# Kernel tuning notes

Hardware: AMD Instinct MI355X
Metric: run time of the kernel (lower is better)

## Reference

```python
import jax, jax.numpy as jnp
import numpy as np

K_NN = 64          # ume_knn
RADIUS = 1.5       # ume_desc_rad
EPS_M = 1e-6
EPS_T = 1e-16


def ball_query_idx(kp, pts, K, radius):
    # kp: [bs, n_kp, 3], pts: [bs, N, 3] -> idx [bs, n_kp, K], -1 padded
    N = pts.shape[1]
    d2 = jnp.sum((kp[:, :, None, :] - pts[:, None, :, :]) ** 2, axis=-1)  # [bs,n_kp,N]
    mask = d2 < radius ** 2
    cand = jnp.where(mask, jnp.arange(N, dtype=jnp.int32), N)
    order = jnp.sort(cand, axis=-1)[..., :K]          # first K in-ball indices (by point index)
    return jnp.where(order == N, -1, order)


def ball_query_gather(pts, idx):
    # pad row 0 with zeros so idx=-1 gathers zeros (matches torch ball_query_gather)
    bs = pts.shape[0]
    padded = jnp.concatenate([jnp.zeros((bs, 1, pts.shape[-1]), pts.dtype), pts], axis=1)
    return padded[jnp.arange(bs)[:, None, None], idx + 1]  # [bs, n_kp, K, D]


def ume_mat(points, features):
    # points: [B', K, 3], features: [B', K, F] -> [B', F, 4]
    m0 = jnp.sum(features, axis=1)                       # [B', F]
    m1 = jnp.einsum('bkf,bkd->bfd', features, points)    # [B', F, 3]
    um = jnp.concatenate([m0[:, :, None], m1], axis=2)   # [B', F, 4]
    denom = jnp.sum(m0, axis=-1)[:, None, None] + EPS_M  # [B',1,1]
    return um / denom


def batch_estimate_transform_ume(G, H):
    # G, H: [B, F, 4]
    mg, mh = G[:, :, 0:1], H[:, :, 0:1]                  # [B,F,1]
    g, h = G[:, :, 1:], H[:, :, 1:]                      # [B,F,3]
    mg_sq = jnp.sum(mg ** 2, axis=1, keepdims=True) + EPS_T
    mg_mh = jnp.sum(mg * mh, axis=1, keepdims=True)
    gmg = jnp.sum(g * mg, axis=1, keepdims=True)         # [B,1,3]
    hmg = jnp.sum(h * mg, axis=1, keepdims=True)
    wlc = gmg / (mg_sq + EPS_T)
    wrc = hmg / (mg_mh + EPS_T)
    left = g - wlc * mg
    right = h - wrc * mh
    M = jnp.einsum('bfi,bfj->bij', right, left)          # right^T @ left, [B,3,3]
    U, S, VH = jnp.linalg.svd(jnp.swapaxes(M, 1, 2))
    sgn = jnp.sign(jnp.linalg.det(U @ VH))
    qd = jnp.stack([jnp.ones_like(sgn), jnp.ones_like(sgn), sgn], axis=-1)  # diag(1,1,sgn)
    R = (U * qd[:, None, :]) @ VH                        # [B,3,3]
    b2 = (wrc - wlc @ R)[:, 0, :]                        # [B,3]
    H_orth = jnp.linalg.qr(H, mode='reduced')[0]
    G_orth = jnp.linalg.qr(G, mode='reduced')[0]
    diff = H_orth @ jnp.swapaxes(H_orth, 1, 2) - G_orth @ jnp.swapaxes(G_orth, 1, 2)
    D = 0.707 * jnp.sqrt(jnp.sum(diff ** 2, axis=(1, 2)))
    top = jnp.concatenate([jnp.swapaxes(R, 1, 2), b2[:, :, None]], axis=2)  # [B,3,4]
    bottom = jnp.broadcast_to(jnp.array([[0.0, 0.0, 0.0, 1.0]], G.dtype), (G.shape[0], 1, 4))
    T = jnp.concatenate([top, bottom], axis=1)           # [B,4,4]
    return T, D


def setup_inputs() -> dict:
    key = jax.random.key(0)
    ks = jax.random.split(key, 6)
    bs, N, F, n_kp = 2, 16384, 64, 64
    return {
        'source_points': jax.random.normal(ks[0], (bs, N, 3), jnp.float32),
        'source_features': jax.random.uniform(ks[1], (bs, N, F), jnp.float32),
        'source_kp': jax.random.normal(ks[2], (bs, n_kp, 3), jnp.float32),
        'target_points': jax.random.normal(ks[3], (bs, N, 3), jnp.float32),
        'target_features': jax.random.uniform(ks[4], (bs, N, F), jnp.float32),
        'target_kp': jax.random.normal(ks[5], (bs, n_kp, 3), jnp.float32),
    }


def reference(source_points, source_features, source_kp, target_points, target_features, target_kp):
    bs, n_kp = source_kp.shape[0], source_kp.shape[1]
    F = source_features.shape[-1]
    s_idx = ball_query_idx(source_kp, source_points, K_NN, RADIUS)
    t_idx = ball_query_idx(target_kp, target_points, K_NN, RADIUS)
    s_pts = ball_query_gather(source_points, s_idx).reshape(bs * n_kp, K_NN, 3)
    s_ft = ball_query_gather(source_features, s_idx).reshape(bs * n_kp, K_NN, F)
    t_pts = ball_query_gather(target_points, t_idx).reshape(bs * n_kp, K_NN, 3)
    t_ft = ball_query_gather(target_features, t_idx).reshape(bs * n_kp, K_NN, F)
    G_kp = ume_mat(s_pts, s_ft).reshape(bs, n_kp, F, 4)[:, :, None]   # [bs,n_kp,1,F,4]
    H_kp = ume_mat(t_pts, t_ft).reshape(bs, n_kp, F, 4)[:, None]      # [bs,1,n_kp,F,4]
    G = jnp.broadcast_to(G_kp, (bs, n_kp, n_kp, F, 4)).reshape(-1, F, 4)
    H = jnp.broadcast_to(H_kp, (bs, n_kp, n_kp, F, 4)).reshape(-1, F, 4)
    T, D = batch_estimate_transform_ume(G, H)
    T = T.reshape(bs, n_kp, n_kp, 4, 4)
    D = D.reshape(bs, n_kp, n_kp)
    return T, D, jnp.squeeze(G_kp), jnp.squeeze(H_kp)
```

## Files before the change

kernel.cpp:

```cpp
#include <hip/hip_runtime.h>
#include <math.h>

#define N_PTS 16384
#define N_KP  64
#define NF    64
#define KNN   64
#define NWAVE 16

#define OFF_T 0
#define OFF_D 131072
#define OFF_G 139264
#define OFF_H 172032

__device__ __forceinline__ float wsum(float v) {
  #pragma unroll
  for (int m = 1; m < 64; m <<= 1) v += __shfl_xor(v, m, 64);
  return v;
}

__global__ __launch_bounds__(1024) void ume_stage1(
    const float* __restrict__ sp, const float* __restrict__ sf, const float* __restrict__ skp,
    const float* __restrict__ tp, const float* __restrict__ tf, const float* __restrict__ tkp,
    float* __restrict__ out, double* __restrict__ rec)
{
  const int kp = blockIdx.x, b = blockIdx.y, side = blockIdx.z;
  const int tid  = threadIdx.x;
  const int lane = tid & 63;
  const int w    = tid >> 6;
  const float* pts  = side ? tp  : sp;
  const float* feat = side ? tf  : sf;
  const float* kps  = side ? tkp : skp;

  const float kx = kps[(b*N_KP + kp)*3 + 0];
  const float ky = kps[(b*N_KP + kp)*3 + 1];
  const float kz = kps[(b*N_KP + kp)*3 + 2];

  __shared__ int   s_widx[NWAVE*KNN];
  __shared__ int   s_wcount[NWAVE];
  __shared__ int   s_woff[NWAVE];
  __shared__ int   s_total;
  __shared__ int   s_final[KNN];
  __shared__ float s_px[KNN], s_py[KNN], s_pz[KNN];
  __shared__ float s_m0[NWAVE][NF], s_mx[NWAVE][NF], s_my[NWAVE][NF], s_mz[NWAVE][NF];

  float px[16], py[16], pz[16];
  const size_t pbase = ((size_t)b*N_PTS + w*1024 + lane)*3;
  #pragma unroll
  for (int k = 0; k < 16; ++k) {
    const float* pp = pts + pbase + (size_t)k*64*3;
    px[k] = pp[0]; py[k] = pp[1]; pz[k] = pp[2];
  }
  int running = 0;
  #pragma unroll
  for (int k = 0; k < 16; ++k) {
    const float dx = px[k]-kx, dy = py[k]-ky, dz = pz[k]-kz;
    const bool hit = (dx*dx + dy*dy + dz*dz) < 2.25f;
    const unsigned long long m = __ballot(hit);
    if (hit) {
      const int pos = running + __popcll(m & ((1ull<<lane)-1ull));
      if (pos < KNN) s_widx[w*KNN + pos] = w*1024 + k*64 + lane;
    }
    running += (int)__popcll(m);
  }
  if (lane == 0) s_wcount[w] = running > KNN ? KNN : running;
  __syncthreads();

  if (tid < NWAVE) {
    int off = 0;
    for (int q = 0; q < tid; ++q) off += s_wcount[q];
    s_woff[tid] = off;
    if (tid == NWAVE-1) {
      int tot = off + s_wcount[tid];
      s_total = tot > KNN ? KNN : tot;
    }
  }
  __syncthreads();

  {
    const int e = tid & 63, ww = tid >> 6;
    if (e < s_wcount[ww]) {
      const int slot = s_woff[ww] + e;
      if (slot < KNN) s_final[slot] = s_widx[ww*KNN + e];
    }
  }
  __syncthreads();

  const int total = s_total;
  if (tid < KNN && tid < total) {
    const float* pp = pts + ((size_t)b*N_PTS + s_final[tid])*3;
    s_px[tid] = pp[0]; s_py[tid] = pp[1]; s_pz[tid] = pp[2];
  }
  __syncthreads();

  {
    const int f = tid & 63, g = tid >> 6;
    float m0 = 0.f, mxv = 0.f, myv = 0.f, mzv = 0.f;
    for (int k = g; k < total; k += NWAVE) {
      const float fv = feat[((size_t)b*N_PTS + s_final[k])*NF + f];
      m0  += fv;
      mxv += fv * s_px[k];
      myv += fv * s_py[k];
      mzv += fv * s_pz[k];
    }
    s_m0[g][f] = m0; s_mx[g][f] = mxv; s_my[g][f] = myv; s_mz[g][f] = mzv;
  }
  __syncthreads();

  if (tid >= 64) return;

  float m0 = 0.f, mxv = 0.f, myv = 0.f, mzv = 0.f;
  #pragma unroll
  for (int g = 0; g < NWAVE; ++g) {
    m0  += s_m0[g][lane];
    mxv += s_mx[g][lane];
    myv += s_my[g][lane];
    mzv += s_mz[g][lane];
  }
  const float denom = wsum(m0) + 1e-6f;
  float u[4];
  u[0] = m0/denom; u[1] = mxv/denom; u[2] = myv/denom; u[3] = mzv/denom;

  float* dst = out + (side ? OFF_H : OFF_G) + ((size_t)(b*N_KP+kp)*NF + lane)*4;
  dst[0]=u[0]; dst[1]=u[1]; dst[2]=u[2]; dst[3]=u[3];

  float A[4][4];
  #pragma unroll
  for (int c = 0; c < 4; ++c)
    #pragma unroll
    for (int d = c; d < 4; ++d) {
      const float s = wsum(u[c]*u[d]);
      A[c][d] = s; A[d][c] = s;
    }

  if (lane < 16)
    rec[(size_t)((side*2 + b)*N_KP + kp)*16 + lane] = (double)A[lane>>2][lane&3];
}

__device__ __forceinline__ void cof_inv4(const double A[4][4], double Ai[4][4], double sc[4]) {
  #pragma unroll
  for (int c = 0; c < 4; ++c) sc[c] = 1.0/sqrt(fmax(A[c][c], 1e-300));
  double M[4][4];
  #pragma unroll
  for (int r = 0; r < 4; ++r)
    #pragma unroll
    for (int c = 0; c < 4; ++c) M[r][c] = A[r][c]*sc[r]*sc[c];
  const double s0 = M[0][0]*M[1][1] - M[0][1]*M[1][0];
  const double s1 = M[0][0]*M[1][2] - M[0][2]*M[1][0];
  const double s2 = M[0][0]*M[1][3] - M[0][3]*M[1][0];
  const double s3 = M[0][1]*M[1][2] - M[0][2]*M[1][1];
  const double s4 = M[0][1]*M[1][3] - M[0][3]*M[1][1];
  const double s5 = M[0][2]*M[1][3] - M[0][3]*M[1][2];
  const double c5 = M[2][2]*M[3][3] - M[2][3]*M[3][2];
  const double c4 = M[2][1]*M[3][3] - M[2][3]*M[3][1];
  const double c3 = M[2][1]*M[3][2] - M[2][2]*M[3][1];
  const double c2 = M[2][0]*M[3][3] - M[2][3]*M[3][0];
  const double c1 = M[2][0]*M[3][2] - M[2][2]*M[3][0];
  const double c0 = M[2][0]*M[3][1] - M[2][1]*M[3][0];
  const double det = s0*c5 - s1*c4 + s2*c3 + s3*c2 - s4*c1 + s5*c0;
  const double invd = 1.0/fmax(det, 1e-300);
  Ai[0][0] = ( M[1][1]*c5 - M[1][2]*c4 + M[1][3]*c3)*invd;
  Ai[0][1] = (-M[0][1]*c5 + M[0][2]*c4 - M[0][3]*c3)*invd;
  Ai[0][2] = ( M[3][1]*s5 - M[3][2]*s4 + M[3][3]*s3)*invd;
  Ai[0][3] = (-M[2][1]*s5 + M[2][2]*s4 - M[2][3]*s3)*invd;
  Ai[1][0] = (-M[1][0]*c5 + M[1][2]*c2 - M[1][3]*c1)*invd;
  Ai[1][1] = ( M[0][0]*c5 - M[0][2]*c2 + M[0][3]*c1)*invd;
  Ai[1][2] = (-M[3][0]*s5 + M[3][2]*s2 - M[3][3]*s1)*invd;
  Ai[1][3] = ( M[2][0]*s5 - M[2][2]*s2 + M[2][3]*s1)*invd;
  Ai[2][0] = ( M[1][0]*c4 - M[1][1]*c2 + M[1][3]*c0)*invd;
  Ai[2][1] = (-M[0][0]*c4 + M[0][1]*c2 - M[0][3]*c0)*invd;
  Ai[2][2] = ( M[3][0]*s4 - M[3][1]*s2 + M[3][3]*s0)*invd;
  Ai[2][3] = (-M[2][0]*s4 + M[2][1]*s2 - M[2][3]*s0)*invd;
  Ai[3][0] = (-M[1][0]*c3 + M[1][1]*c1 - M[1][2]*c0)*invd;
  Ai[3][1] = ( M[0][0]*c3 - M[0][1]*c1 + M[0][2]*c0)*invd;
  Ai[3][2] = (-M[3][0]*s3 + M[3][1]*s1 - M[3][2]*s0)*invd;
  Ai[3][3] = ( M[2][0]*s3 - M[2][1]*s1 + M[2][2]*s0)*invd;
}

__global__ __launch_bounds__(256) void ume_stage2(
    const float* __restrict__ gh, float* __restrict__ out,
    const double* __restrict__ rec)
{
  const int q  = blockIdx.x*256 + threadIdx.x;
  const int b2 = q >> 12;
  const int i  = (q >> 6) & 63;
  const int j  = q & 63;

  const float4* Gp = (const float4*)(gh + OFF_G) + (size_t)(b2*N_KP + i)*NF;
  const float4* Hp = (const float4*)(gh + OFF_H) + (size_t)(b2*N_KP + j)*NF;

  double X[4][4] = {};
  for (int f = 0; f < NF; ++f) {
    const float4 g = Gp[f];
    const float4 h = Hp[f];
    const double gc[4] = {(double)g.x, (double)g.y, (double)g.z, (double)g.w};
    const double hc[4] = {(double)h.x, (double)h.y, (double)h.z, (double)h.w};
    #pragma unroll
    for (int c = 0; c < 4; ++c)
      #pragma unroll
      for (int d = 0; d < 4; ++d)
        X[c][d] += hc[c]*gc[d];
  }

  double Ag[4][4], Bh[4][4];
  {
    const double* pg = rec + (size_t)(b2*N_KP + i)*16;
    const double* ph = rec + (size_t)((2 + b2)*N_KP + j)*16;
    #pragma unroll
    for (int k = 0; k < 16; ++k) { Ag[k>>2][k&3] = pg[k]; Bh[k>>2][k&3] = ph[k]; }
  }
  double Aig[4][4], scg[4], Bih[4][4], sch[4];
  cof_inv4(Ag, Aig, scg);
  cof_inv4(Bh, Bih, sch);

  const double inv_dwl = 1.0/(Ag[0][0] + 2e-16);
  const double wl[3] = {Ag[0][1]*inv_dwl, Ag[0][2]*inv_dwl, Ag[0][3]*inv_dwl};
  const double inv_dmm = 1.0/(X[0][0] + 1e-16);
  const double wr[3] = {X[1][0]*inv_dmm, X[2][0]*inv_dmm, X[3][0]*inv_dmm};

  double M3[3][3];
  #pragma unroll
  for (int r = 0; r < 3; ++r)
    #pragma unroll
    for (int c = 0; c < 3; ++c)
      M3[r][c] = X[1+r][1+c] - wl[c]*X[1+r][0] - wr[r]*X[0][1+c] + wr[r]*wl[c]*X[0][0];

  double C[3][3];
  for (int r = 0; r < 3; ++r)
    for (int c = 0; c < 3; ++c) C[r][c] = M3[c][r];

  double mmax = 0.0;
  for (int r = 0; r < 3; ++r)
    for (int c = 0; c < 3; ++c) mmax = fmax(mmax, fabs(C[r][c]));

  double R[3][3] = {{1,0,0},{0,1,0},{0,0,1}};
  if (mmax > 1e-300) {
    const double is = 1.0/mmax;
    for (int r = 0; r < 3; ++r)
      for (int c = 0; c < 3; ++c) C[r][c] *= is;
    double K[3][3];
    for (int p = 0; p < 3; ++p)
      for (int qq = 0; qq < 3; ++qq) {
        double s = 0.0;
        for (int r = 0; r < 3; ++r) s += C[r][p]*C[r][qq];
        K[p][qq] = s;
      }
    double V[3][3] = {{1,0,0},{0,1,0},{0,0,1}};
    for (int sweep = 0; sweep < 5; ++sweep) {
      for (int p = 0; p < 2; ++p)
        for (int qq = p+1; qq < 3; ++qq) {
          const double apq = K[p][qq];
          if (apq*apq < 1e-26) continue;
          const double tau = (K[qq][qq] - K[p][p])/(2.0*apq);
          const double t   = (tau >= 0.0 ? 1.0 : -1.0)/(fabs(tau) + sqrt(1.0 + tau*tau));
          const double cth = 1.0/sqrt(1.0 + t*t);
          const double sth = t*cth;
          for (int k = 0; k < 3; ++k) {
            const double a = K[p][k], bb_ = K[qq][k];
            K[p][k] = cth*a - sth*bb_;
            K[qq][k] = sth*a + cth*bb_;
          }
          for (int k = 0; k < 3; ++k) {
            const double a = K[k][p], bb_ = K[k][qq];
            K[k][p] = cth*a - sth*bb_;
            K[k][qq] = sth*a + cth*bb_;
          }
          for (int k = 0; k < 3; ++k) {
            const double a = V[k][p], bb_ = V[k][qq];
            V[k][p] = cth*a - sth*bb_;
            V[k][qq] = sth*a + cth*bb_;
          }
        }
    }
    int o0 = 0, o1 = 1, o2 = 2;
    double e0 = K[0][0], e1 = K[1][1], e2 = K[2][2];
    if (e0 < e1) { double te=e0; e0=e1; e1=te; int to=o0; o0=o1; o1=to; }
    if (e0 < e2) { double te=e0; e0=e2; e2=te; int to=o0; o0=o2; o2=to; }
    if (e1 < e2) { double te=e1; e1=e2; e2=te; int to=o1; o1=o2; o2=to; }
    (void)e0; (void)e1; (void)e2;
    double v1[3] = {V[0][o0], V[1][o0], V[2][o0]};
    double v2[3] = {V[0][o1], V[1][o1], V[2][o1]};
    double u1[3], u2[3];
    for (int r = 0; r < 3; ++r) u1[r] = C[r][0]*v1[0] + C[r][1]*v1[1] + C[r][2]*v1[2];
    const double n1 = sqrt(u1[0]*u1[0] + u1[1]*u1[1] + u1[2]*u1[2]);
    if (n1 > 1e-150) { const double rn = 1.0/n1; u1[0]*=rn; u1[1]*=rn; u1[2]*=rn; }
    else             { u1[0]=1.0; u1[1]=0.0; u1[2]=0.0; }
    for (int r = 0; r < 3; ++r) u2[r] = C[r][0]*v2[0] + C[r][1]*v2[1] + C[r][2]*v2[2];
    const double d12 = u2[0]*u1[0] + u2[1]*u1[1] + u2[2]*u1[2];
    for (int r = 0; r < 3; ++r) u2[r] -= d12*u1[r];
    const double n2 = sqrt(u2[0]*u2[0] + u2[1]*u2[1] + u2[2]*u2[2]);
    if (n2 > 1e-100) { const double rn = 1.0/n2; u2[0]*=rn; u2[1]*=rn; u2[2]*=rn; }
    else {
      double t0, t1, t2;
      if (fabs(u1[0]) < 0.9) { t0=1.0; t1=0.0; t2=0.0; } else { t0=0.0; t1=1.0; t2=0.0; }
      const double dd = t0*u1[0] + t1*u1[1] + t2*u1[2];
      u2[0]=t0-dd*u1[0]; u2[1]=t1-dd*u1[1]; u2[2]=t2-dd*u1[2];
      const double nn = 1.0/sqrt(u2[0]*u2[0] + u2[1]*u2[1] + u2[2]*u2[2]);
      u2[0]*=nn; u2[1]*=nn; u2[2]*=nn;
    }
    const double u3[3] = {u1[1]*u2[2]-u1[2]*u2[1], u1[2]*u2[0]-u1[0]*u2[2], u1[0]*u2[1]-u1[1]*u2[0]};
    const double v3[3] = {v1[1]*v2[2]-v1[2]*v2[1], v1[2]*v2[0]-v1[0]*v2[2], v1[0]*v2[1]-v1[1]*v2[0]};
    for (int r = 0; r < 3; ++r)
      for (int c = 0; c < 3; ++c)
        R[r][c] = u1[r]*v1[c] + u2[r]*v2[c] + u3[r]*v3[c];
  }

  double bb[3];
  for (int d = 0; d < 3; ++d)
    bb[d] = wr[d] - (wl[0]*R[0][d] + wl[1]*R[1][d] + wl[2]*R[2][d]);

  double Xh[4][4];
  for (int c = 0; c < 4; ++c)
    for (int d = 0; d < 4; ++d) Xh[c][d] = X[c][d]*sch[c]*scg[d];
  double W[4][4];
  for (int r = 0; r < 4; ++r)
    for (int c = 0; c < 4; ++c) {
      double s = 0.0;
      for (int k = 0; k < 4; ++k) s += Bih[r][k]*Xh[k][c];
      W[r][c] = s;
    }
  double tr = 0.0;
  for (int r = 0; r < 4; ++r)
    for (int c = 0; c < 4; ++c) {
      double s = 0.0;
      for (int k = 0; k < 4; ++k) s += W[r][k]*Aig[k][c];
      tr += s*Xh[r][c];
    }
  const double Dv = 0.707*sqrt(fmax(8.0 - 2.0*tr, 0.0));

  float* tptr = out + OFF_T + (size_t)((b2*N_KP + i)*N_KP + j)*16;
  tptr[0]=(float)R[0][0];  tptr[1]=(float)R[1][0];  tptr[2]=(float)R[2][0];  tptr[3]=(float)bb[0];
  tptr[4]=(float)R[0][1];  tptr[5]=(float)R[1][1];  tptr[6]=(float)R[2][1];  tptr[7]=(float)bb[1];
  tptr[8]=(float)R[0][2];  tptr[9]=(float)R[1][2];  tptr[10]=(float)R[2][2]; tptr[11]=(float)bb[2];
  tptr[12]=0.f; tptr[13]=0.f; tptr[14]=0.f; tptr[15]=1.f;

  out[OFF_D + (size_t)(b2*N_KP + i)*N_KP + j] = (float)Dv;
}

extern "C" void kernel_launch(void* const* d_in, const int* in_sizes, int n_in,
                              void* d_out, int out_size, void* d_ws, size_t ws_size,
                              hipStream_t stream) {
  const float* sp  = (const float*)d_in[0];
  const float* sf  = (const float*)d_in[1];
  const float* skp = (const float*)d_in[2];
  const float* tp  = (const float*)d_in[3];
  const float* tf  = (const float*)d_in[4];
  const float* tkp = (const float*)d_in[5];
  float* out = (float*)d_out;
  double* rec = (double*)d_ws;

  dim3 gA(N_KP, 2, 2);
  ume_stage1<<<gA, 1024, 0, stream>>>(sp, sf, skp, tp, tf, tkp, out, rec);
  ume_stage2<<<32, 256, 0, stream>>>(out, out, rec);
}
```

Measured before the change: 98.43 us.

## Precompute per-keypoint 4x4 inverses once and tile stage2 into 8x8 pair blocks

Moves the two cofactor 4x4 inversions and the wl weights out of every (i,j) pair thread into a small ume_invert kernel that runs once per keypoint and stores the results in workspace. Stage2 then reads these precomputed records instead of redoing the inversions 64 times each. Stage2 also changes from 32 blocks of 256 threads to 128 blocks of 64 threads covering 8x8 pair tiles, which spreads work over more CUs and lets G/H rows be reused within a block. The cost is an extra kernel launch and a serial dependency, plus extra global reads of the double records.

```diff
diff --git a/kernel.cpp b/kernel.cpp
--- a/kernel.cpp
+++ b/kernel.cpp
@@ -11,6 +11,8 @@
 #define OFF_D 131072
 #define OFF_G 139264
 #define OFF_H 172032
+
+#define REC2_OFF 4096
 
 __device__ __forceinline__ float wsum(float v) {
   #pragma unroll
@@ -176,17 +178,38 @@
   Ai[3][3] = ( M[2][0]*s3 - M[2][1]*s1 + M[2][2]*s0)*invd;
 }
 
-__global__ __launch_bounds__(256) void ume_stage2(
+__global__ __launch_bounds__(64) void ume_invert(double* __restrict__ ws)
+{
+  const int t = blockIdx.x*64 + threadIdx.x;
+  if (t >= 256) return;
+  const double* pa = ws + (size_t)t*16;
+  double A[4][4];
+  #pragma unroll
+  for (int k = 0; k < 16; ++k) A[k>>2][k&3] = pa[k];
+  double Ai[4][4], sc[4];
+  cof_inv4(A, Ai, sc);
+  double* rp = ws + REC2_OFF + (size_t)t*24;
+  #pragma unroll
+  for (int k = 0; k < 16; ++k) rp[k] = Ai[k>>2][k&3];
+  rp[16]=sc[0]; rp[17]=sc[1]; rp[18]=sc[2]; rp[19]=sc[3];
+  const double inv_dwl = 1.0/(A[0][0] + 2e-16);
+  rp[20] = A[0][1]*inv_dwl;
+  rp[21] = A[0][2]*inv_dwl;
+  rp[22] = A[0][3]*inv_dwl;
+  rp[23] = 0.0;
+}
+
+__global__ __launch_bounds__(64) void ume_stage2(
     const float* __restrict__ gh, float* __restrict__ out,
-    const double* __restrict__ rec)
+    const double* __restrict__ rec2)
 {
-  const int q  = blockIdx.x*256 + threadIdx.x;
-  const int b2 = q >> 12;
-  const int i  = (q >> 6) & 63;
-  const int j  = q & 63;
-
-  const float4* Gp = (const float4*)(gh + OFF_G) + (size_t)(b2*N_KP + i)*NF;
-  const float4* Hp = (const float4*)(gh + OFF_H) + (size_t)(b2*N_KP + j)*NF;
+  const int jt = blockIdx.x, it = blockIdx.y, b = blockIdx.z;
+  const int lane = threadIdx.x;
+  const int i = it*8 + (lane >> 3);
+  const int j = jt*8 + (lane & 7);
+
+  const float4* Gp = (const float4*)(gh + OFF_G) + (size_t)(b*N_KP + i)*NF;
+  const float4* Hp = (const float4*)(gh + OFF_H) + (size_t)(b*N_KP + j)*NF;
 
   double X[4][4] = {};
   for (int f = 0; f < NF; ++f) {
@@ -201,32 +224,23 @@
         X[c][d] += hc[c]*gc[d];
   }
 
-  double Ag[4][4], Bh[4][4];
-  {
-    const double* pg = rec + (size_t)(b2*N_KP + i)*16;
-    const double* ph = rec + (size_t)((2 + b2)*N_KP + j)*16;
-    #pragma unroll
-    for (int k = 0; k < 16; ++k) { Ag[k>>2][k&3] = pg[k]; Bh[k>>2][k&3] = ph[k]; }
-  }
-  double Aig[4][4], scg[4], Bih[4][4], sch[4];
-  cof_inv4(Ag, Aig, scg);
-  cof_inv4(Bh, Bih, sch);
-
-  const double inv_dwl = 1.0/(Ag[0][0] + 2e-16);
-  const double wl[3] = {Ag[0][1]*inv_dwl, Ag[0][2]*inv_dwl, Ag[0][3]*inv_dwl};
+  const double* rg = rec2 + (size_t)(b*N_KP + i)*24;
+  const double* rh = rec2 + (size_t)((2 + b)*N_KP + j)*24;
+
+  const double wl[3] = {rg[20], rg[21], rg[22]};
   const double inv_dmm = 1.0/(X[0][0] + 1e-16);
   const double wr[3] = {X[1][0]*inv_dmm, X[2][0]*inv_dmm, X[3][0]*inv_dmm};
 
-  double M3[3][3];
+  double M[3][3];
   #pragma unroll
   for (int r = 0; r < 3; ++r)
     #pragma unroll
     for (int c = 0; c < 3; ++c)
-      M3[r][c] = X[1+r][1+c] - wl[c]*X[1+r][0] - wr[r]*X[0][1+c] + wr[r]*wl[c]*X[0][0];
+      M[r][c] = X[1+r][1+c] - wl[c]*X[1+r][0] - wr[r]*X[0][1+c] + wr[r]*wl[c]*X[0][0];
 
   double C[3][3];
   for (int r = 0; r < 3; ++r)
-    for (int c = 0; c < 3; ++c) C[r][c] = M3[c][r];
+    for (int c = 0; c < 3; ++c) C[r][c] = M[c][r];
 
   double mmax = 0.0;
   for (int r = 0; r < 3; ++r)
@@ -239,35 +253,35 @@
       for (int c = 0; c < 3; ++c) C[r][c] *= is;
     double K[3][3];
     for (int p = 0; p < 3; ++p)
-      for (int qq = 0; qq < 3; ++qq) {
+      for (int q = 0; q < 3; ++q) {
         double s = 0.0;
-        for (int r = 0; r < 3; ++r) s += C[r][p]*C[r][qq];
-        K[p][qq] = s;
+        for (int r = 0; r < 3; ++r) s += C[r][p]*C[r][q];
+        K[p][q] = s;
       }
     double V[3][3] = {{1,0,0},{0,1,0},{0,0,1}};
     for (int sweep = 0; sweep < 5; ++sweep) {
       for (int p = 0; p < 2; ++p)
-        for (int qq = p+1; qq < 3; ++qq) {
-          const double apq = K[p][qq];
+        for (int q = p+1; q < 3; ++q) {
+          const double apq = K[p][q];
           if (apq*apq < 1e-26) continue;
-          const double tau = (K[qq][qq] - K[p][p])/(2.0*apq);
+          const double tau = (K[q][q] - K[p][p])/(2.0*apq);
           const double t   = (tau >= 0.0 ? 1.0 : -1.0)/(fabs(tau) + sqrt(1.0 + tau*tau));
           const double cth = 1.0/sqrt(1.0 + t*t);
           const double sth = t*cth;
           for (int k = 0; k < 3; ++k) {
-            const double a = K[p][k], bb_ = K[qq][k];
+            const double a = K[p][k], bb_ = K[q][k];
             K[p][k] = cth*a - sth*bb_;
-            K[qq][k] = sth*a + cth*bb_;
+            K[q][k] = sth*a + cth*bb_;
           }
           for (int k = 0; k < 3; ++k) {
-            const double a = K[k][p], bb_ = K[k][qq];
+            const double a = K[k][p], bb_ = K[k][q];
             K[k][p] = cth*a - sth*bb_;
-            K[k][qq] = sth*a + cth*bb_;
+            K[k][q] = sth*a + cth*bb_;
           }
           for (int k = 0; k < 3; ++k) {
-            const double a = V[k][p], bb_ = V[k][qq];
+            const double a = V[k][p], bb_ = V[k][q];
             V[k][p] = cth*a - sth*bb_;
-            V[k][qq] = sth*a + cth*bb_;
+            V[k][q] = sth*a + cth*bb_;
           }
         }
     }
@@ -308,32 +322,34 @@
   for (int d = 0; d < 3; ++d)
     bb[d] = wr[d] - (wl[0]*R[0][d] + wl[1]*R[1][d] + wl[2]*R[2][d]);
 
+  const double sg[4] = {rg[16], rg[17], rg[18], rg[19]};
+  const double sh[4] = {rh[16], rh[17], rh[18], rh[19]};
   double Xh[4][4];
   for (int c = 0; c < 4; ++c)
-    for (int d = 0; d < 4; ++d) Xh[c][d] = X[c][d]*sch[c]*scg[d];
+    for (int d = 0; d < 4; ++d) Xh[c][d] = X[c][d]*sh[c]*sg[d];
   double W[4][4];
   for (int r = 0; r < 4; ++r)
     for (int c = 0; c < 4; ++c) {
       double s = 0.0;
-      for (int k = 0; k < 4; ++k) s += Bih[r][k]*Xh[k][c];
+      for (int k = 0; k < 4; ++k) s += rh[r*4+k]*Xh[k][c];
       W[r][c] = s;
     }
   double tr = 0.0;
   for (int r = 0; r < 4; ++r)
     for (int c = 0; c < 4; ++c) {
       double s = 0.0;
-      for (int k = 0; k < 4; ++k) s += W[r][k]*Aig[k][c];
+      for (int k = 0; k < 4; ++k) s += W[r][k]*rg[k*4+c];
       tr += s*Xh[r][c];
     }
   const double Dv = 0.707*sqrt(fmax(8.0 - 2.0*tr, 0.0));
 
-  float* tptr = out + OFF_T + (size_t)((b2*N_KP + i)*N_KP + j)*16;
+  float* tptr = out + OFF_T + (size_t)((b*N_KP + i)*N_KP + j)*16;
   tptr[0]=(float)R[0][0];  tptr[1]=(float)R[1][0];  tptr[2]=(float)R[2][0];  tptr[3]=(float)bb[0];
   tptr[4]=(float)R[0][1];  tptr[5]=(float)R[1][1];  tptr[6]=(float)R[2][1];  tptr[7]=(float)bb[1];
   tptr[8]=(float)R[0][2];  tptr[9]=(float)R[1][2];  tptr[10]=(float)R[2][2]; tptr[11]=(float)bb[2];
   tptr[12]=0.f; tptr[13]=0.f; tptr[14]=0.f; tptr[15]=1.f;
 
-  out[OFF_D + (size_t)(b2*N_KP + i)*N_KP + j] = (float)Dv;
+  out[OFF_D + (size_t)(b*N_KP + i)*N_KP + j] = (float)Dv;
 }
 
 extern "C" void kernel_launch(void* const* d_in, const int* in_sizes, int n_in,
@@ -346,9 +362,11 @@
   const float* tf  = (const float*)d_in[4];
   const float* tkp = (const float*)d_in[5];
   float* out = (float*)d_out;
-  double* rec = (double*)d_ws;
+  double* ws = (double*)d_ws;
 
   dim3 gA(N_KP, 2, 2);
-  ume_stage1<<<gA, 1024, 0, stream>>>(sp, sf, skp, tp, tf, tkp, out, rec);
-  ume_stage2<<<32, 256, 0, stream>>>(out, out, rec);
-}
+  ume_stage1<<<gA, 1024, 0, stream>>>(sp, sf, skp, tp, tf, tkp, out, ws);
+  ume_invert<<<4, 64, 0, stream>>>(ws);
+  dim3 gB(8, 8, 2);
+  ume_stage2<<<gB, 64, 0, stream>>>(out, out, ws + REC2_OFF);
+}
```

After: 108.7 us. 10.4% more time.
